# Performance work log

Hardware: AMD Instinct MI355X
Metric: run time of the kernel (lower is better)

## Reference

```python
import jax, jax.numpy as jnp
import numpy as np


def setup_inputs() -> dict:
    key = jax.random.key(0)
    k1, k2 = jax.random.split(key)
    B, N1, N2, D = 256, 32, 32, 512
    ner_j = jax.random.normal(k1, (B, N1, D), dtype=jnp.float32)
    face_j = jax.random.normal(k2, (B, N2, D), dtype=jnp.float32)
    return {"face_j": face_j, "ner_j": ner_j}


def reference(face_j, ner_j):
    # torch.matmul(ner_j.unsqueeze(1), face_j.permute(0,2,1)) broadcasts to the
    # pairwise score tensor: scores[b, c, n, f] = <ner_j[b, n], face_j[c, f]>
    scores = jnp.einsum('bnd,cfd->bcnf', ner_j, face_j)  # (B, B, N1, N2)
    # mean over num_spans2 then mean over num_spans1 (sum + div in original)
    logits = scores.mean(axis=-1).mean(axis=-1)           # (B, B)
    # cross_entropy(logits, targets=arange(B)) with mean reduction
    logp = jax.nn.log_softmax(logits, axis=-1)
    diag = jnp.diagonal(logp)                             # logp[b, b]
    return -jnp.mean(diag)
```

## Files before the change

### kernel.cpp

```cpp
#include <hip/hip_runtime.h>
#include <hip/hip_bf16.h>

#define BB 256
#define NN 32
#define DD 512
#define ROWS 4

__global__ __launch_bounds__(256) void reduce_sums(
    const float* __restrict__ ner, const float* __restrict__ face,
    float* __restrict__ u, float* __restrict__ vT, float* __restrict__ out) {
  int idx = blockIdx.x * 256 + threadIdx.x;
  if (idx == 0) out[0] = 0.0f;
  const int half = BB * DD / 4;
  bool is_ner = idx < half;
  int j = is_ner ? idx : idx - half;
  int row = j >> 7;
  int d4  = j & 127;
  const float* src = is_ner ? ner : face;
  const float4* p = (const float4*)(src + (size_t)row * NN * DD) + d4;
  float4 s = make_float4(0.f, 0.f, 0.f, 0.f);
#pragma unroll
  for (int n = 0; n < NN; ++n) {
    float4 x = p[n * (DD / 4)];
    s.x += x.x; s.y += x.y; s.z += x.z; s.w += x.w;
  }
  if (is_ner) {
    ((float4*)(u + (size_t)row * DD))[d4] = s;
  } else {
    int d = d4 * 4;
    vT[(size_t)(d + 0) * BB + row] = s.x;
    vT[(size_t)(d + 1) * BB + row] = s.y;
    vT[(size_t)(d + 2) * BB + row] = s.z;
    vT[(size_t)(d + 3) * BB + row] = s.w;
  }
}

__global__ __launch_bounds__(256) void row_lse4(
    const float* __restrict__ u, const float* __restrict__ vT,
    float* __restrict__ out) {
  const int b0 = blockIdx.x * ROWS;
  const int t = threadIdx.x;
  __shared__ float us[ROWS * DD];
  __shared__ float ls[ROWS][BB];
  __shared__ float wsum[ROWS];

  const float4* usrc = (const float4*)(u + (size_t)b0 * DD);
#pragma unroll
  for (int i = 0; i < (ROWS * DD / 4) / 256; ++i)
    ((float4*)us)[t + i * 256] = usrc[t + i * 256];
  __syncthreads();

  float acc0 = 0.f, acc1 = 0.f, acc2 = 0.f, acc3 = 0.f;
#pragma unroll 8
  for (int d = 0; d < DD; ++d) {
    float v = vT[(size_t)d * BB + t];
    acc0 = fmaf(us[0 * DD + d], v, acc0);
    acc1 = fmaf(us[1 * DD + d], v, acc1);
    acc2 = fmaf(us[2 * DD + d], v, acc2);
    acc3 = fmaf(us[3 * DD + d], v, acc3);
  }
  const float sc = 1.f / (NN * NN);
  ls[0][t] = acc0 * sc;
  ls[1][t] = acc1 * sc;
  ls[2][t] = acc2 * sc;
  ls[3][t] = acc3 * sc;
  __syncthreads();

  const int w = t >> 6;
  const int lane = t & 63;
  float x0 = ls[w][lane];
  float x1 = ls[w][lane + 64];
  float x2 = ls[w][lane + 128];
  float x3 = ls[w][lane + 192];
  float m = fmaxf(fmaxf(x0, x1), fmaxf(x2, x3));
#pragma unroll
  for (int off = 32; off > 0; off >>= 1) m = fmaxf(m, __shfl_xor(m, off, 64));
  float e = __expf(x0 - m) + __expf(x1 - m) + __expf(x2 - m) + __expf(x3 - m);
#pragma unroll
  for (int off = 32; off > 0; off >>= 1) e += __shfl_xor(e, off, 64);
  if (lane == 0) {
    float lse = m + __logf(e);
    float diag = ls[w][b0 + w];
    wsum[w] = diag - lse;
  }
  __syncthreads();
  if (t == 0) {
    atomicAdd(out, -(wsum[0] + wsum[1] + wsum[2] + wsum[3]) * (1.f / BB));
  }
}

extern "C" void kernel_launch(void* const* d_in, const int* in_sizes, int n_in,
                              void* d_out, int out_size, void* d_ws, size_t ws_size,
                              hipStream_t stream) {
  const float* face = (const float*)d_in[0];
  const float* ner  = (const float*)d_in[1];
  float* u  = (float*)d_ws;
  float* vT = u + (size_t)BB * DD;
  float* out = (float*)d_out;

  const int total_threads = 2 * BB * DD / 4;
  reduce_sums<<<total_threads / 256, 256, 0, stream>>>(ner, face, u, vT, out);
  row_lse4<<<BB / ROWS, 256, 0, stream>>>(u, vT, out);
}
```

Measured before the change: 95.09 us.

## Store face sums as packed bf16 and split logits reduction across K

The per-batch face sums are written transposed as packed bf16 pairs, halving the bytes the logits kernel streams. The logits kernel now handles two rows per block with 1024 threads, splitting the 512-wide dot product four ways and combining partials in shared memory. This is meant to raise occupancy and cut latency-bound serial loads, at the cost of bf16 rounding error in the logits.

```diff
diff --git a/kernel.cpp b/kernel.cpp
--- a/kernel.cpp
+++ b/kernel.cpp
@@ -4,11 +4,18 @@
 #define BB 256
 #define NN 32
 #define DD 512
-#define ROWS 4
+#define ROWS 2
+#define KSPLIT 4
+
+static __device__ inline unsigned f2bf(float x) {
+  union { float f; unsigned u; } a; a.f = x;
+  unsigned r = a.u + 0x7fff + ((a.u >> 16) & 1);
+  return r >> 16;
+}
 
 __global__ __launch_bounds__(256) void reduce_sums(
     const float* __restrict__ ner, const float* __restrict__ face,
-    float* __restrict__ u, float* __restrict__ vT, float* __restrict__ out) {
+    float* __restrict__ u, unsigned* __restrict__ vTp, float* __restrict__ out) {
   int idx = blockIdx.x * 256 + threadIdx.x;
   if (idx == 0) out[0] = 0.0f;
   const int half = BB * DD / 4;
@@ -27,66 +34,69 @@
   if (is_ner) {
     ((float4*)(u + (size_t)row * DD))[d4] = s;
   } else {
-    int d = d4 * 4;
-    vT[(size_t)(d + 0) * BB + row] = s.x;
-    vT[(size_t)(d + 1) * BB + row] = s.y;
-    vT[(size_t)(d + 2) * BB + row] = s.z;
-    vT[(size_t)(d + 3) * BB + row] = s.w;
+    int dp0 = 2 * d4;
+    vTp[(size_t)dp0 * BB + row]       = (f2bf(s.y) << 16) | f2bf(s.x);
+    vTp[(size_t)(dp0 + 1) * BB + row] = (f2bf(s.w) << 16) | f2bf(s.z);
   }
 }
 
-__global__ __launch_bounds__(256) void row_lse4(
-    const float* __restrict__ u, const float* __restrict__ vT,
+__global__ __launch_bounds__(1024) void row_lse_bf16(
+    const float* __restrict__ u, const unsigned* __restrict__ vTp,
     float* __restrict__ out) {
   const int b0 = blockIdx.x * ROWS;
   const int t = threadIdx.x;
+  const int c = t & 255;
+  const int k = t >> 8;
   __shared__ float us[ROWS * DD];
-  __shared__ float ls[ROWS][BB];
+  __shared__ float ls[KSPLIT][ROWS][BB];
+  __shared__ float lg[ROWS][BB];
   __shared__ float wsum[ROWS];
 
-  const float4* usrc = (const float4*)(u + (size_t)b0 * DD);
-#pragma unroll
-  for (int i = 0; i < (ROWS * DD / 4) / 256; ++i)
-    ((float4*)us)[t + i * 256] = usrc[t + i * 256];
+  if (t < ROWS * DD / 4)
+    ((float4*)us)[t] = ((const float4*)(u + (size_t)b0 * DD))[t];
   __syncthreads();
 
-  float acc0 = 0.f, acc1 = 0.f, acc2 = 0.f, acc3 = 0.f;
+  float a0l = 0.f, a0h = 0.f, a1l = 0.f, a1h = 0.f;
+  const unsigned* p = vTp + (size_t)(k * (DD / 2 / KSPLIT)) * BB + c;
+  const float* u0 = us + k * (DD / KSPLIT);
+  const float* u1 = us + DD + k * (DD / KSPLIT);
 #pragma unroll 8
-  for (int d = 0; d < DD; ++d) {
-    float v = vT[(size_t)d * BB + t];
-    acc0 = fmaf(us[0 * DD + d], v, acc0);
-    acc1 = fmaf(us[1 * DD + d], v, acc1);
-    acc2 = fmaf(us[2 * DD + d], v, acc2);
-    acc3 = fmaf(us[3 * DD + d], v, acc3);
+  for (int i = 0; i < DD / 2 / KSPLIT; ++i) {
+    unsigned w = p[(size_t)i * BB];
+    float vlo = __uint_as_float(w << 16);
+    float vhi = __uint_as_float(w & 0xffff0000u);
+    a0l = fmaf(u0[2 * i],     vlo, a0l);
+    a0h = fmaf(u0[2 * i + 1], vhi, a0h);
+    a1l = fmaf(u1[2 * i],     vlo, a1l);
+    a1h = fmaf(u1[2 * i + 1], vhi, a1h);
   }
-  const float sc = 1.f / (NN * NN);
-  ls[0][t] = acc0 * sc;
-  ls[1][t] = acc1 * sc;
-  ls[2][t] = acc2 * sc;
-  ls[3][t] = acc3 * sc;
+  ls[k][0][c] = a0l + a0h;
+  ls[k][1][c] = a1l + a1h;
   __syncthreads();
 
-  const int w = t >> 6;
-  const int lane = t & 63;
-  float x0 = ls[w][lane];
-  float x1 = ls[w][lane + 64];
-  float x2 = ls[w][lane + 128];
-  float x3 = ls[w][lane + 192];
-  float m = fmaxf(fmaxf(x0, x1), fmaxf(x2, x3));
-#pragma unroll
-  for (int off = 32; off > 0; off >>= 1) m = fmaxf(m, __shfl_xor(m, off, 64));
-  float e = __expf(x0 - m) + __expf(x1 - m) + __expf(x2 - m) + __expf(x3 - m);
-#pragma unroll
-  for (int off = 32; off > 0; off >>= 1) e += __shfl_xor(e, off, 64);
-  if (lane == 0) {
-    float lse = m + __logf(e);
-    float diag = ls[w][b0 + w];
-    wsum[w] = diag - lse;
+  const float sc = 1.f / (NN * NN);
+  if (t < ROWS * BB) {
+    int cc = t & 255, r = t >> 8;
+    lg[r][cc] = (ls[0][r][cc] + ls[1][r][cc] + ls[2][r][cc] + ls[3][r][cc]) * sc;
   }
   __syncthreads();
-  if (t == 0) {
-    atomicAdd(out, -(wsum[0] + wsum[1] + wsum[2] + wsum[3]) * (1.f / BB));
+
+  const int wv = t >> 6, lane = t & 63;
+  if (wv < ROWS) {
+    float x0 = lg[wv][lane];
+    float x1 = lg[wv][lane + 64];
+    float x2 = lg[wv][lane + 128];
+    float x3 = lg[wv][lane + 192];
+    float m = fmaxf(fmaxf(x0, x1), fmaxf(x2, x3));
+#pragma unroll
+    for (int off = 32; off > 0; off >>= 1) m = fmaxf(m, __shfl_xor(m, off, 64));
+    float e = __expf(x0 - m) + __expf(x1 - m) + __expf(x2 - m) + __expf(x3 - m);
+#pragma unroll
+    for (int off = 32; off > 0; off >>= 1) e += __shfl_xor(e, off, 64);
+    if (lane == 0) wsum[wv] = lg[wv][b0 + wv] - (m + __logf(e));
   }
+  __syncthreads();
+  if (t == 0) atomicAdd(out, -(wsum[0] + wsum[1]) * (1.f / BB));
 }
 
 extern "C" void kernel_launch(void* const* d_in, const int* in_sizes, int n_in,
@@ -94,11 +104,11 @@
                               hipStream_t stream) {
   const float* face = (const float*)d_in[0];
   const float* ner  = (const float*)d_in[1];
-  float* u  = (float*)d_ws;
-  float* vT = u + (size_t)BB * DD;
+  float* u = (float*)d_ws;
+  unsigned* vTp = (unsigned*)(u + (size_t)BB * DD);
   float* out = (float*)d_out;
 
   const int total_threads = 2 * BB * DD / 4;
-  reduce_sums<<<total_threads / 256, 256, 0, stream>>>(ner, face, u, vT, out);
-  row_lse4<<<BB / ROWS, 256, 0, stream>>>(u, vT, out);
+  reduce_sums<<<total_threads / 256, 256, 0, stream>>>(ner, face, u, vTp, out);
+  row_lse_bf16<<<BB / ROWS, 1024, 0, stream>>>(u, vTp, out);
 }
```

Measured after the change: 81.13 us. 1.17x faster.
